# Optimization experiments

Hardware: AMD Instinct MI355X
Metric: run time of the kernel (lower is better)

The kernel has to match this reference:

```python
import jax, jax.numpy as jnp
import numpy as np

WINDOW = 11
SIGMA = 1.5
CHANNELS = 3
C1 = 0.01 ** 2
C2 = 0.03 ** 2


def _gaussian_kernel(size=WINDOW, sigma=SIGMA, channels=CHANNELS):
    coords = jnp.arange(size, dtype=jnp.float32) - size // 2
    g = jnp.exp(-coords ** 2 / (2.0 * sigma ** 2))
    g = jnp.outer(g, g)
    g = g / g.sum()
    # depthwise kernel: [C, 1, K, K] (OIHW with feature_group_count=C)
    return jnp.broadcast_to(g[None, None], (channels, 1, size, size))


def _dwconv(x, kernel):
    # x: [N, C, H, W]; SAME padding, depthwise (groups = C)
    pad = WINDOW // 2
    return jax.lax.conv_general_dilated(
        x, kernel,
        window_strides=(1, 1),
        padding=[(pad, pad), (pad, pad)],
        dimension_numbers=('NCHW', 'OIHW', 'NCHW'),
        feature_group_count=CHANNELS,
    )


def setup_inputs() -> dict:
    key = jax.random.key(0)
    k1, k2 = jax.random.split(key)
    shape = (16, 3, 512, 512)
    pred = jax.random.uniform(k1, shape, dtype=jnp.float32)
    target = jax.random.uniform(k2, shape, dtype=jnp.float32)
    return {"pred": pred, "target": target}


def reference(pred, target):
    kernel = _gaussian_kernel().astype(pred.dtype)
    mu_p = _dwconv(pred, kernel)
    mu_t = _dwconv(target, kernel)
    mu_p2 = mu_p * mu_p
    mu_t2 = mu_t * mu_t
    mu_pt = mu_p * mu_t
    sigma_p2 = _dwconv(pred * pred, kernel) - mu_p2
    sigma_t2 = _dwconv(target * target, kernel) - mu_t2
    sigma_pt = _dwconv(pred * target, kernel) - mu_pt
    ssim_map = ((2.0 * mu_pt + C1) * (2.0 * sigma_pt + C2)) / (
        (mu_p2 + mu_t2 + C1) * (sigma_p2 + sigma_t2 + C2)
    )
    return 1.0 - ssim_map.mean()
```

## Files before the change

kernel.cpp:

```cpp
#include <hip/hip_runtime.h>
#include <math.h>

#define IMG_H 512
#define IMG_W 512
#define TILE  32
#define NSLOT 64
#define SAB_R 48
#define SAB_S 56
#define HT_S  56

typedef _Float16 f16x4 __attribute__((ext_vector_type(4)));
typedef _Float16 f16x8 __attribute__((ext_vector_type(8)));
typedef float    f32x4 __attribute__((ext_vector_type(4)));

union F16Frag { f16x8 v8; f16x4 v4[2]; };

__global__ __launch_bounds__(256, 5)
void ssim_main(const float* __restrict__ pred, const float* __restrict__ targ,
               float* __restrict__ partial, double* __restrict__ acc, int mode)
{
    __shared__ _Float16 frags[2][64][8];
    __shared__ _Float16 sAB[2][SAB_R][SAB_S];
    __shared__ _Float16 hT[5][TILE][HT_S];

    const int tid  = threadIdx.x;
    const int lane = tid & 63;
    const int wave = tid >> 6;
    const int ln   = lane & 15;
    const int lg   = lane >> 4;

    const int tx = blockIdx.x, ty = blockIdx.y, img = blockIdx.z;
    const float* __restrict__ p = pred + (size_t)img * (IMG_H * IMG_W);
    const float* __restrict__ t = targ + (size_t)img * (IMG_H * IMG_W);
    const int gr0 = ty * TILE - 5;
    const int wo  = tx * TILE - 8;

    if (tid < 128) {
        const int which = tid >> 6, l = tid & 63;
        const int lln = l & 15, llg = l >> 4;
        f16x8 f;
        #pragma unroll
        for (int j = 0; j < 8; ++j) {
            int k   = llg * 8 + j;
            int idx = which ? (k - lln) : (k - lln - 3);
            float d = (float)(idx - 5);
            float v = 0.26601173f * exp2f(-d * d * 0.32059889f);
            f[j] = (_Float16)(((unsigned)idx <= 10u) ? v : 0.0f);
        }
        *(f16x8*)&frags[which][l][0] = f;
    }

    for (int i = tid; i < SAB_R * 6; i += 256) {
        const int r = i / 6, g = i - 6 * r;
        const int gr = gr0 + r;
        const bool in = (gr >= 0) && (gr < IMG_H) &&
                        !(tx == 0 && g == 0) && !(tx == 15 && g == 5);
        float4 p0 = {0,0,0,0}, p1 = {0,0,0,0}, t0 = {0,0,0,0}, t1 = {0,0,0,0};
        if (in) {
            const float* bp = p + (size_t)gr * IMG_W + (wo + 8 * g);
            const float* bt = t + (size_t)gr * IMG_W + (wo + 8 * g);
            p0 = ((const float4*)bp)[0]; p1 = ((const float4*)bp)[1];
            t0 = ((const float4*)bt)[0]; t1 = ((const float4*)bt)[1];
        }
        *(f16x8*)&sAB[0][r][8 * g] =
            f16x8{(_Float16)p0.x, (_Float16)p0.y, (_Float16)p0.z, (_Float16)p0.w,
                  (_Float16)p1.x, (_Float16)p1.y, (_Float16)p1.z, (_Float16)p1.w};
        *(f16x8*)&sAB[1][r][8 * g] =
            f16x8{(_Float16)t0.x, (_Float16)t0.y, (_Float16)t0.z, (_Float16)t0.w,
                  (_Float16)t1.x, (_Float16)t1.y, (_Float16)t1.z, (_Float16)t1.w};
    }
    __syncthreads();

    const f16x8 Bw  = *(const f16x8*)&frags[0][lane][0];
    const f16x8 A2w = *(const f16x8*)&frags[1][lane][0];
    const f32x4 zacc = {0.f, 0.f, 0.f, 0.f};

    auto do_tile = [&](int tt) {
        const int rt = tt >> 1, ct = tt & 1;
        const int rowbase = rt * 16;
        const int arow = rowbase + ln;
        const int acol = ct * 16 + lg * 8;
        F16Frag pa, ta;
        pa.v8 = *(const f16x8*)&sAB[0][arow][acol];
        ta.v8 = *(const f16x8*)&sAB[1][arow][acol];
        f16x8 fq[5];
        fq[0] = pa.v8;
        fq[1] = ta.v8;
        fq[2] = pa.v8 * pa.v8;
        fq[3] = ta.v8 * ta.v8;
        fq[4] = pa.v8 * ta.v8;
        const int ocol = ct * 16 + ln;
        const int orow = rowbase + lg * 4;
        #pragma unroll
        for (int q = 0; q < 5; ++q) {
            f32x4 d = __builtin_amdgcn_mfma_f32_16x16x32_f16(fq[q], Bw, zacc, 0, 0, 0);
            *(f16x4*)&hT[q][ocol][orow] =
                f16x4{(_Float16)d[0], (_Float16)d[1], (_Float16)d[2], (_Float16)d[3]};
        }
    };
    do_tile(wave);
    if (wave < 2) do_tile(wave + 4);
    __syncthreads();

    float lsum = 0.f;
    {
        const int ctv = wave & 1, rtv = wave >> 1;
        const int ocol  = ctv * 16 + ln;
        const int rbase = rtv * 16 + lg * 8;
        f32x4 accq[5];
        #pragma unroll
        for (int q = 0; q < 5; ++q) {
            f16x8 b = *(const f16x8*)&hT[q][ocol][rbase];
            accq[q] = __builtin_amdgcn_mfma_f32_16x16x32_f16(A2w, b, zacc, 0, 0, 0);
        }
        const float C1 = 1e-4f, C2 = 9e-4f;
        #pragma unroll
        for (int rgi = 0; rgi < 4; ++rgi) {
            float mp = accq[0][rgi], mt = accq[1][rgi];
            float vp = accq[2][rgi] - mp * mp;
            float vt = accq[3][rgi] - mt * mt;
            float cv = accq[4][rgi] - mp * mt;
            float num = (2.f * mp * mt + C1) * (2.f * cv + C2);
            float den = (mp * mp + mt * mt + C1) * (vp + vt + C2);
            lsum = fmaf(num, __builtin_amdgcn_rcpf(den), lsum);
        }
    }

    #pragma unroll
    for (int off = 32; off > 0; off >>= 1)
        lsum += __shfl_down(lsum, off, 64);
    if (lane == 0) {
        const int bid = (blockIdx.z * gridDim.y + blockIdx.y) * gridDim.x + blockIdx.x;
        if (mode == 0) {
            partial[bid * 4 + wave] = lsum;
        } else {
            atomicAdd(&acc[(bid * 4 + wave) & (NSLOT - 1)], (double)lsum);
        }
    }
}

__global__ void ssim_init(double* acc)
{
    if (threadIdx.x < NSLOT) acc[threadIdx.x] = 0.0;
}

__global__ __launch_bounds__(1024)
void ssim_fin_slots(const float* __restrict__ partial, float* __restrict__ out,
                    int n4, double inv_n)
{
    __shared__ double red[16];
    double s = 0.0;
    const int tid = threadIdx.x;
    for (int i = tid; i < n4; i += 1024) {
        float4 v = ((const float4*)partial)[i];
        s += (double)v.x + (double)v.y + (double)v.z + (double)v.w;
    }
    #pragma unroll
    for (int off = 32; off > 0; off >>= 1)
        s += __shfl_down(s, off, 64);
    if ((tid & 63) == 0) red[tid >> 6] = s;
    __syncthreads();
    if (tid == 0) {
        double tot = 0.0;
        #pragma unroll
        for (int w = 0; w < 16; ++w) tot += red[w];
        out[0] = (float)(1.0 - tot * inv_n);
    }
}

__global__ void ssim_fin_atomic(const double* __restrict__ acc, float* __restrict__ out,
                                double inv_n)
{
    if (threadIdx.x == 0) {
        double s = 0.0;
        for (int i = 0; i < NSLOT; ++i) s += acc[i];
        out[0] = (float)(1.0 - s * inv_n);
    }
}

extern "C" void kernel_launch(void* const* d_in, const int* in_sizes, int n_in,
                              void* d_out, int out_size, void* d_ws, size_t ws_size,
                              hipStream_t stream)
{
    const float* pred = (const float*)d_in[0];
    const float* targ = (const float*)d_in[1];
    float* out = (float*)d_out;

    const long long total = (long long)in_sizes[0];
    const int n_img = (int)(total / (IMG_H * IMG_W));
    dim3 grid(IMG_W / TILE, IMG_H / TILE, n_img);
    const int nblk = grid.x * grid.y * grid.z;
    const int nslots = nblk * 4;
    const double inv_n = 1.0 / (double)total;

    if (ws_size >= (size_t)nslots * sizeof(float)) {
        float* partial = (float*)d_ws;
        hipLaunchKernelGGL(ssim_main, grid, dim3(256), 0, stream,
                           pred, targ, partial, (double*)nullptr, 0);
        hipLaunchKernelGGL(ssim_fin_slots, dim3(1), dim3(1024), 0, stream,
                           partial, out, nslots / 4, inv_n);
    } else {
        double* acc = (double*)d_ws;
        hipLaunchKernelGGL(ssim_init, dim3(1), dim3(64), 0, stream, acc);
        hipLaunchKernelGGL(ssim_main, grid, dim3(256), 0, stream,
                           pred, targ, (float*)nullptr, acc, 1);
        hipLaunchKernelGGL(ssim_fin_atomic, dim3(1), dim3(1), 0, stream,
                           acc, out, inv_n);
    }
}
```

Measured before the change: 145.8 us.

## Load SSIM input tiles straight into registers and drop block barriers

Removes the shared-memory staging buffer for the input tiles. Each wave now loads its own fp16 MFMA operand fragments directly from global memory and writes horizontal-pass results into a wave-private region of the transposed buffer, so both __syncthreads are gone. The Gaussian weight fragments are built once by a small init kernel, and the occupancy hint is raised from 5 to 6. In exchange, the two row-parity waves redundantly compute the overlapping 16-row band, there is one extra kernel launch, and correctness relies on each wave reading only LDS rows it wrote itself, which it does.

Measured after the change: 156.9 us. +7.7%, slower.

```diff
diff --git a/kernel.cpp b/kernel.cpp
--- a/kernel.cpp
+++ b/kernel.cpp
@@ -3,123 +3,107 @@
 
 #define IMG_H 512
 #define IMG_W 512
-#define TILE  32
 #define NSLOT 64
-#define SAB_R 48
-#define SAB_S 56
-#define HT_S  56
+#define HT_R  56
 
 typedef _Float16 f16x4 __attribute__((ext_vector_type(4)));
 typedef _Float16 f16x8 __attribute__((ext_vector_type(8)));
 typedef float    f32x4 __attribute__((ext_vector_type(4)));
 
-union F16Frag { f16x8 v8; f16x4 v4[2]; };
+__device__ __forceinline__ f16x8 pack8(const float4& a, const float4& b) {
+    return f16x8{(_Float16)a.x, (_Float16)a.y, (_Float16)a.z, (_Float16)a.w,
+                 (_Float16)b.x, (_Float16)b.y, (_Float16)b.z, (_Float16)b.w};
+}
 
-__global__ __launch_bounds__(256, 5)
+__device__ __forceinline__ f16x8 build_frag(int which, int l)
+{
+    const int lln = l & 15, llg = l >> 4;
+    f16x8 f;
+    #pragma unroll
+    for (int j = 0; j < 8; ++j) {
+        int idx = llg * 8 + j - lln - (which ? 0 : 3);
+        float d = (float)(idx - 5);
+        float v = 0.26601173f * exp2f(-d * d * 0.32059889f);
+        f[j] = (_Float16)(((unsigned)idx <= 10u) ? v : 0.0f);
+    }
+    return f;
+}
+
+__global__ void ssim_frag_init(f16x8* __restrict__ frags)
+{
+    const int tid = threadIdx.x;
+    if (tid < 128) frags[tid] = build_frag(tid >> 6, tid & 63);
+}
+
+__global__ __launch_bounds__(256, 6)
 void ssim_main(const float* __restrict__ pred, const float* __restrict__ targ,
-               float* __restrict__ partial, double* __restrict__ acc, int mode)
+               const f16x8* __restrict__ frags, float* __restrict__ partial,
+               double* __restrict__ acc, int mode)
 {
-    __shared__ _Float16 frags[2][64][8];
-    __shared__ _Float16 sAB[2][SAB_R][SAB_S];
-    __shared__ _Float16 hT[5][TILE][HT_S];
+    __shared__ _Float16 hT[2][5][16][HT_R];
 
     const int tid  = threadIdx.x;
-    const int lane = tid & 63;
-    const int wave = tid >> 6;
-    const int ln   = lane & 15;
-    const int lg   = lane >> 4;
+    const int lane = tid & 63, wave = tid >> 6;
+    const int ln   = lane & 15, lg = lane >> 4;
+    const int ct   = wave >> 1, par = wave & 1;
 
     const int tx = blockIdx.x, ty = blockIdx.y, img = blockIdx.z;
     const float* __restrict__ p = pred + (size_t)img * (IMG_H * IMG_W);
     const float* __restrict__ t = targ + (size_t)img * (IMG_H * IMG_W);
-    const int gr0 = ty * TILE - 5;
-    const int wo  = tx * TILE - 8;
 
-    if (tid < 128) {
-        const int which = tid >> 6, l = tid & 63;
-        const int lln = l & 15, llg = l >> 4;
-        f16x8 f;
-        #pragma unroll
-        for (int j = 0; j < 8; ++j) {
-            int k   = llg * 8 + j;
-            int idx = which ? (k - lln) : (k - lln - 3);
-            float d = (float)(idx - 5);
-            float v = 0.26601173f * exp2f(-d * d * 0.32059889f);
-            f[j] = (_Float16)(((unsigned)idx <= 10u) ? v : 0.0f);
+    f16x8 Bw, A2w;
+    if (frags) { Bw = frags[lane]; A2w = frags[64 + lane]; }
+    else       { Bw = build_frag(0, lane); A2w = build_frag(1, lane); }
+
+    const int rb0 = par ? 16 : 0;
+    const int gc  = tx * 32 + ct * 16 + lg * 8 - 8;
+    const bool colOK = (gc >= 0) && (gc <= IMG_W - 8);
+    float4 P[2][2] = {}, T[2][2] = {};
+    #pragma unroll
+    for (int pos = 0; pos < 2; ++pos) {
+        const int gr = ty * 32 - 5 + rb0 + 16 * pos + ln;
+        if (colOK && gr >= 0 && gr < IMG_H) {
+            const float* bp = p + (size_t)gr * IMG_W + gc;
+            const float* bt = t + (size_t)gr * IMG_W + gc;
+            P[pos][0] = ((const float4*)bp)[0];  P[pos][1] = ((const float4*)bp)[1];
+            T[pos][0] = ((const float4*)bt)[0];  T[pos][1] = ((const float4*)bt)[1];
         }
-        *(f16x8*)&frags[which][l][0] = f;
     }
+    const f32x4 z = {0.f, 0.f, 0.f, 0.f};
 
-    for (int i = tid; i < SAB_R * 6; i += 256) {
-        const int r = i / 6, g = i - 6 * r;
-        const int gr = gr0 + r;
-        const bool in = (gr >= 0) && (gr < IMG_H) &&
-                        !(tx == 0 && g == 0) && !(tx == 15 && g == 5);
-        float4 p0 = {0,0,0,0}, p1 = {0,0,0,0}, t0 = {0,0,0,0}, t1 = {0,0,0,0};
-        if (in) {
-            const float* bp = p + (size_t)gr * IMG_W + (wo + 8 * g);
-            const float* bt = t + (size_t)gr * IMG_W + (wo + 8 * g);
-            p0 = ((const float4*)bp)[0]; p1 = ((const float4*)bp)[1];
-            t0 = ((const float4*)bt)[0]; t1 = ((const float4*)bt)[1];
-        }
-        *(f16x8*)&sAB[0][r][8 * g] =
-            f16x8{(_Float16)p0.x, (_Float16)p0.y, (_Float16)p0.z, (_Float16)p0.w,
-                  (_Float16)p1.x, (_Float16)p1.y, (_Float16)p1.z, (_Float16)p1.w};
-        *(f16x8*)&sAB[1][r][8 * g] =
-            f16x8{(_Float16)t0.x, (_Float16)t0.y, (_Float16)t0.z, (_Float16)t0.w,
-                  (_Float16)t1.x, (_Float16)t1.y, (_Float16)t1.z, (_Float16)t1.w};
-    }
-    __syncthreads();
-
-    const f16x8 Bw  = *(const f16x8*)&frags[0][lane][0];
-    const f16x8 A2w = *(const f16x8*)&frags[1][lane][0];
-    const f32x4 zacc = {0.f, 0.f, 0.f, 0.f};
-
-    auto do_tile = [&](int tt) {
-        const int rt = tt >> 1, ct = tt & 1;
-        const int rowbase = rt * 16;
-        const int arow = rowbase + ln;
-        const int acol = ct * 16 + lg * 8;
-        F16Frag pa, ta;
-        pa.v8 = *(const f16x8*)&sAB[0][arow][acol];
-        ta.v8 = *(const f16x8*)&sAB[1][arow][acol];
+    #pragma unroll
+    for (int pos = 0; pos < 2; ++pos) {
+        const int rowbase = rb0 + 16 * pos;
+        f16x8 pa = pack8(P[pos][0], P[pos][1]);
+        f16x8 ta = pack8(T[pos][0], T[pos][1]);
         f16x8 fq[5];
-        fq[0] = pa.v8;
-        fq[1] = ta.v8;
-        fq[2] = pa.v8 * pa.v8;
-        fq[3] = ta.v8 * ta.v8;
-        fq[4] = pa.v8 * ta.v8;
-        const int ocol = ct * 16 + ln;
+        fq[0] = pa; fq[1] = ta;
+        fq[2] = pa * pa; fq[3] = ta * ta; fq[4] = pa * ta;
         const int orow = rowbase + lg * 4;
         #pragma unroll
         for (int q = 0; q < 5; ++q) {
-            f32x4 d = __builtin_amdgcn_mfma_f32_16x16x32_f16(fq[q], Bw, zacc, 0, 0, 0);
-            *(f16x4*)&hT[q][ocol][orow] =
+            f32x4 d = __builtin_amdgcn_mfma_f32_16x16x32_f16(fq[q], Bw, z, 0, 0, 0);
+            *(f16x4*)&hT[ct][q][ln][orow] =
                 f16x4{(_Float16)d[0], (_Float16)d[1], (_Float16)d[2], (_Float16)d[3]};
         }
-    };
-    do_tile(wave);
-    if (wave < 2) do_tile(wave + 4);
-    __syncthreads();
+    }
 
     float lsum = 0.f;
     {
-        const int ctv = wave & 1, rtv = wave >> 1;
-        const int ocol  = ctv * 16 + ln;
-        const int rbase = rtv * 16 + lg * 8;
+        const int rbase = par * 16 + lg * 8;
         f32x4 accq[5];
         #pragma unroll
         for (int q = 0; q < 5; ++q) {
-            f16x8 b = *(const f16x8*)&hT[q][ocol][rbase];
-            accq[q] = __builtin_amdgcn_mfma_f32_16x16x32_f16(A2w, b, zacc, 0, 0, 0);
+            f16x8 b = *(const f16x8*)&hT[ct][q][ln][rbase];
+            accq[q] = __builtin_amdgcn_mfma_f32_16x16x32_f16(A2w, b, z, 0, 0, 0);
         }
         const float C1 = 1e-4f, C2 = 9e-4f;
         #pragma unroll
-        for (int rgi = 0; rgi < 4; ++rgi) {
-            float mp = accq[0][rgi], mt = accq[1][rgi];
-            float vp = accq[2][rgi] - mp * mp;
-            float vt = accq[3][rgi] - mt * mt;
-            float cv = accq[4][rgi] - mp * mt;
+        for (int r = 0; r < 4; ++r) {
+            float mp = accq[0][r], mt = accq[1][r];
+            float vp = accq[2][r] - mp * mp;
+            float vt = accq[3][r] - mt * mt;
+            float cv = accq[4][r] - mp * mt;
             float num = (2.f * mp * mt + C1) * (2.f * cv + C2);
             float den = (mp * mp + mt * mt + C1) * (vp + vt + C2);
             lsum = fmaf(num, __builtin_amdgcn_rcpf(den), lsum);
@@ -131,11 +115,8 @@
         lsum += __shfl_down(lsum, off, 64);
     if (lane == 0) {
         const int bid = (blockIdx.z * gridDim.y + blockIdx.y) * gridDim.x + blockIdx.x;
-        if (mode == 0) {
-            partial[bid * 4 + wave] = lsum;
-        } else {
-            atomicAdd(&acc[(bid * 4 + wave) & (NSLOT - 1)], (double)lsum);
-        }
+        if (mode == 0) partial[bid * 4 + wave] = lsum;
+        else atomicAdd(&acc[(bid * 4 + wave) & (NSLOT - 1)], (double)lsum);
     }
 }
 
@@ -188,22 +169,25 @@
 
     const long long total = (long long)in_sizes[0];
     const int n_img = (int)(total / (IMG_H * IMG_W));
-    dim3 grid(IMG_W / TILE, IMG_H / TILE, n_img);
+    dim3 grid(IMG_W / 32, IMG_H / 32, n_img);
     const int nblk = grid.x * grid.y * grid.z;
     const int nslots = nblk * 4;
     const double inv_n = 1.0 / (double)total;
+    const size_t fragBytes = 128 * sizeof(f16x8);
 
-    if (ws_size >= (size_t)nslots * sizeof(float)) {
-        float* partial = (float*)d_ws;
+    if (ws_size >= fragBytes + (size_t)nslots * sizeof(float)) {
+        f16x8* frags   = (f16x8*)d_ws;
+        float* partial = (float*)((char*)d_ws + fragBytes);
+        hipLaunchKernelGGL(ssim_frag_init, dim3(1), dim3(128), 0, stream, frags);
         hipLaunchKernelGGL(ssim_main, grid, dim3(256), 0, stream,
-                           pred, targ, partial, (double*)nullptr, 0);
+                           pred, targ, (const f16x8*)frags, partial, (double*)nullptr, 0);
         hipLaunchKernelGGL(ssim_fin_slots, dim3(1), dim3(1024), 0, stream,
                            partial, out, nslots / 4, inv_n);
     } else {
         double* acc = (double*)d_ws;
         hipLaunchKernelGGL(ssim_init, dim3(1), dim3(64), 0, stream, acc);
         hipLaunchKernelGGL(ssim_main, grid, dim3(256), 0, stream,
-                           pred, targ, (float*)nullptr, acc, 1);
+                           pred, targ, (const f16x8*)nullptr, (float*)nullptr, acc, 1);
         hipLaunchKernelGGL(ssim_fin_atomic, dim3(1), dim3(1), 0, stream,
                            acc, out, inv_n);
     }
```

## Use sum/difference basis to cut SSIM convolutions from five to four

Applied to the files above, without the earlier changes.

Loads pred+target and pred-target into shared memory and convolves S, D, S² and D², which gives the same SSIM terms with four filtered quantities instead of five. This removes one MFMA pass per stage and a fifth of the transposed intermediate LDS buffer, so occupancy is raised to 6 blocks. The Gaussian fragments are now built in registers per lane instead of staged through LDS. The change of basis adds fp16 cancellation risk when forming the covariance and variance from differences.

Measured after the change: 140.3 us. 1.04x faster.

```diff
diff --git a/kernel.cpp b/kernel.cpp
--- a/kernel.cpp
+++ b/kernel.cpp
@@ -3,9 +3,7 @@
 
 #define IMG_H 512
 #define IMG_W 512
-#define TILE  32
 #define NSLOT 64
-#define SAB_R 48
 #define SAB_S 56
 #define HT_S  56
 
@@ -13,44 +11,42 @@
 typedef _Float16 f16x8 __attribute__((ext_vector_type(8)));
 typedef float    f32x4 __attribute__((ext_vector_type(4)));
 
-union F16Frag { f16x8 v8; f16x4 v4[2]; };
-
-__global__ __launch_bounds__(256, 5)
+__device__ __forceinline__ f16x8 build_frag(int which, int l)
+{
+    const int lln = l & 15, llg = l >> 4;
+    f16x8 f;
+    #pragma unroll
+    for (int j = 0; j < 8; ++j) {
+        int idx = llg * 8 + j - lln - (which ? 0 : 3);
+        float d = (float)(idx - 5);
+        float v = 0.26601173f * exp2f(-d * d * 0.32059889f);
+        f[j] = (_Float16)(((unsigned)idx <= 10u) ? v : 0.0f);
+    }
+    return f;
+}
+
+__global__ __launch_bounds__(256, 6)
 void ssim_main(const float* __restrict__ pred, const float* __restrict__ targ,
                float* __restrict__ partial, double* __restrict__ acc, int mode)
 {
-    __shared__ _Float16 frags[2][64][8];
-    __shared__ _Float16 sAB[2][SAB_R][SAB_S];
-    __shared__ _Float16 hT[5][TILE][HT_S];
+    __shared__ _Float16 sAB[2][48][SAB_S];
+    __shared__ _Float16 hT[4][32][HT_S];
 
     const int tid  = threadIdx.x;
-    const int lane = tid & 63;
-    const int wave = tid >> 6;
-    const int ln   = lane & 15;
-    const int lg   = lane >> 4;
+    const int lane = tid & 63, wave = tid >> 6;
+    const int ln   = lane & 15, lg = lane >> 4;
 
     const int tx = blockIdx.x, ty = blockIdx.y, img = blockIdx.z;
     const float* __restrict__ p = pred + (size_t)img * (IMG_H * IMG_W);
     const float* __restrict__ t = targ + (size_t)img * (IMG_H * IMG_W);
-    const int gr0 = ty * TILE - 5;
-    const int wo  = tx * TILE - 8;
-
-    if (tid < 128) {
-        const int which = tid >> 6, l = tid & 63;
-        const int lln = l & 15, llg = l >> 4;
-        f16x8 f;
-        #pragma unroll
-        for (int j = 0; j < 8; ++j) {
-            int k   = llg * 8 + j;
-            int idx = which ? (k - lln) : (k - lln - 3);
-            float d = (float)(idx - 5);
-            float v = 0.26601173f * exp2f(-d * d * 0.32059889f);
-            f[j] = (_Float16)(((unsigned)idx <= 10u) ? v : 0.0f);
-        }
-        *(f16x8*)&frags[which][l][0] = f;
-    }
-
-    for (int i = tid; i < SAB_R * 6; i += 256) {
+    const int gr0 = ty * 32 - 5;
+    const int wo  = tx * 32 - 8;
+
+    const f16x8 Bw  = build_frag(0, lane);
+    const f16x8 A2w = build_frag(1, lane);
+    const f32x4 z = {0.f, 0.f, 0.f, 0.f};
+
+    for (int i = tid; i < 48 * 6; i += 256) {
         const int r = i / 6, g = i - 6 * r;
         const int gr = gr0 + r;
         const bool in = (gr >= 0) && (gr < IMG_H) &&
@@ -62,40 +58,34 @@
             p0 = ((const float4*)bp)[0]; p1 = ((const float4*)bp)[1];
             t0 = ((const float4*)bt)[0]; t1 = ((const float4*)bt)[1];
         }
-        *(f16x8*)&sAB[0][r][8 * g] =
-            f16x8{(_Float16)p0.x, (_Float16)p0.y, (_Float16)p0.z, (_Float16)p0.w,
-                  (_Float16)p1.x, (_Float16)p1.y, (_Float16)p1.z, (_Float16)p1.w};
-        *(f16x8*)&sAB[1][r][8 * g] =
-            f16x8{(_Float16)t0.x, (_Float16)t0.y, (_Float16)t0.z, (_Float16)t0.w,
-                  (_Float16)t1.x, (_Float16)t1.y, (_Float16)t1.z, (_Float16)t1.w};
+        *(f16x8*)&sAB[0][r][8 * g] = f16x8{
+            (_Float16)(p0.x + t0.x), (_Float16)(p0.y + t0.y),
+            (_Float16)(p0.z + t0.z), (_Float16)(p0.w + t0.w),
+            (_Float16)(p1.x + t1.x), (_Float16)(p1.y + t1.y),
+            (_Float16)(p1.z + t1.z), (_Float16)(p1.w + t1.w)};
+        *(f16x8*)&sAB[1][r][8 * g] = f16x8{
+            (_Float16)(p0.x - t0.x), (_Float16)(p0.y - t0.y),
+            (_Float16)(p0.z - t0.z), (_Float16)(p0.w - t0.w),
+            (_Float16)(p1.x - t1.x), (_Float16)(p1.y - t1.y),
+            (_Float16)(p1.z - t1.z), (_Float16)(p1.w - t1.w)};
     }
     __syncthreads();
-
-    const f16x8 Bw  = *(const f16x8*)&frags[0][lane][0];
-    const f16x8 A2w = *(const f16x8*)&frags[1][lane][0];
-    const f32x4 zacc = {0.f, 0.f, 0.f, 0.f};
 
     auto do_tile = [&](int tt) {
         const int rt = tt >> 1, ct = tt & 1;
         const int rowbase = rt * 16;
-        const int arow = rowbase + ln;
-        const int acol = ct * 16 + lg * 8;
-        F16Frag pa, ta;
-        pa.v8 = *(const f16x8*)&sAB[0][arow][acol];
-        ta.v8 = *(const f16x8*)&sAB[1][arow][acol];
-        f16x8 fq[5];
-        fq[0] = pa.v8;
-        fq[1] = ta.v8;
-        fq[2] = pa.v8 * pa.v8;
-        fq[3] = ta.v8 * ta.v8;
-        fq[4] = pa.v8 * ta.v8;
+        f16x8 s8 = *(const f16x8*)&sAB[0][rowbase + ln][ct * 16 + lg * 8];
+        f16x8 d8 = *(const f16x8*)&sAB[1][rowbase + ln][ct * 16 + lg * 8];
+        f16x8 fq[4];
+        fq[0] = s8; fq[1] = d8;
+        fq[2] = s8 * s8; fq[3] = d8 * d8;
         const int ocol = ct * 16 + ln;
         const int orow = rowbase + lg * 4;
         #pragma unroll
-        for (int q = 0; q < 5; ++q) {
-            f32x4 d = __builtin_amdgcn_mfma_f32_16x16x32_f16(fq[q], Bw, zacc, 0, 0, 0);
+        for (int q = 0; q < 4; ++q) {
+            f32x4 dd = __builtin_amdgcn_mfma_f32_16x16x32_f16(fq[q], Bw, z, 0, 0, 0);
             *(f16x4*)&hT[q][ocol][orow] =
-                f16x4{(_Float16)d[0], (_Float16)d[1], (_Float16)d[2], (_Float16)d[3]};
+                f16x4{(_Float16)dd[0], (_Float16)dd[1], (_Float16)dd[2], (_Float16)dd[3]};
         }
     };
     do_tile(wave);
@@ -107,21 +97,24 @@
         const int ctv = wave & 1, rtv = wave >> 1;
         const int ocol  = ctv * 16 + ln;
         const int rbase = rtv * 16 + lg * 8;
-        f32x4 accq[5];
-        #pragma unroll
-        for (int q = 0; q < 5; ++q) {
+        f32x4 accq[4];
+        #pragma unroll
+        for (int q = 0; q < 4; ++q) {
             f16x8 b = *(const f16x8*)&hT[q][ocol][rbase];
-            accq[q] = __builtin_amdgcn_mfma_f32_16x16x32_f16(A2w, b, zacc, 0, 0, 0);
+            accq[q] = __builtin_amdgcn_mfma_f32_16x16x32_f16(A2w, b, z, 0, 0, 0);
         }
         const float C1 = 1e-4f, C2 = 9e-4f;
         #pragma unroll
-        for (int rgi = 0; rgi < 4; ++rgi) {
-            float mp = accq[0][rgi], mt = accq[1][rgi];
-            float vp = accq[2][rgi] - mp * mp;
-            float vt = accq[3][rgi] - mt * mt;
-            float cv = accq[4][rgi] - mp * mt;
-            float num = (2.f * mp * mt + C1) * (2.f * cv + C2);
-            float den = (mp * mp + mt * mt + C1) * (vp + vt + C2);
+        for (int r = 0; r < 4; ++r) {
+            float F1 = accq[0][r], F2 = accq[1][r];
+            float F3 = accq[2][r], F4 = accq[3][r];
+            float a = F1 * F1, b = F2 * F2;
+            float mpmt2 = 0.5f * (a - b);
+            float msq   = 0.5f * (a + b);
+            float cpt2  = 0.5f * (F3 - F4) - mpmt2;
+            float vsum  = 0.5f * (F3 + F4) - msq;
+            float num = (mpmt2 + C1) * (cpt2 + C2);
+            float den = (msq + C1) * (vsum + C2);
             lsum = fmaf(num, __builtin_amdgcn_rcpf(den), lsum);
         }
     }
@@ -131,11 +124,8 @@
         lsum += __shfl_down(lsum, off, 64);
     if (lane == 0) {
         const int bid = (blockIdx.z * gridDim.y + blockIdx.y) * gridDim.x + blockIdx.x;
-        if (mode == 0) {
-            partial[bid * 4 + wave] = lsum;
-        } else {
-            atomicAdd(&acc[(bid * 4 + wave) & (NSLOT - 1)], (double)lsum);
-        }
+        if (mode == 0) partial[bid * 4 + wave] = lsum;
+        else atomicAdd(&acc[(bid * 4 + wave) & (NSLOT - 1)], (double)lsum);
     }
 }
 
@@ -188,7 +178,7 @@
 
     const long long total = (long long)in_sizes[0];
     const int n_img = (int)(total / (IMG_H * IMG_W));
-    dim3 grid(IMG_W / TILE, IMG_H / TILE, n_img);
+    dim3 grid(IMG_W / 32, IMG_H / 32, n_img);
     const int nblk = grid.x * grid.y * grid.z;
     const int nslots = nblk * 4;
     const double inv_n = 1.0 / (double)total;
```
